# Optimization experiments

Hardware: AMD Instinct MI355X
Metric: run time of the kernel (lower is better)

Reference implementation:

```python
import jax, jax.numpy as jnp
import numpy as np
import math

B, N, DMODEL, H = 8, 1024, 256, 8
HEAD_DIM = DMODEL // H


def setup_inputs() -> dict:
    key = jax.random.key(0)
    ks = jax.random.split(key, 8)
    x = jax.random.normal(ks[0], (B, N, DMODEL), dtype=jnp.float32)
    # symmetric-ish nonnegative pairwise distances
    adj = jax.random.uniform(ks[1], (B, N, N), dtype=jnp.float32) * 10.0
    mask = jax.random.uniform(ks[2], (B, N)) < 0.9  # bool, mostly valid nodes
    W_qkv = jax.random.normal(ks[3], (DMODEL, 3 * DMODEL), dtype=jnp.float32) / math.sqrt(DMODEL)
    b_qkv = jax.random.normal(ks[4], (3 * DMODEL,), dtype=jnp.float32) * 0.01
    shifts = jnp.arange(1.0, H + 1.0, dtype=jnp.float32)  # initial_shifts
    widths = jnp.ones((H,), dtype=jnp.float32)            # initial_widths
    # self_loop_W = 1/head_dim + U(0,1), non-trainable
    self_loop_w = 1.0 / HEAD_DIM + jax.random.uniform(ks[5], (H,), dtype=jnp.float32)
    return {"x": x, "adj": adj, "mask": mask, "W_qkv": W_qkv, "b_qkv": b_qkv,
            "shifts": shifts, "widths": widths, "self_loop_w": self_loop_w}


def reference(x, adj, mask, W_qkv, b_qkv, shifts, widths, self_loop_w):
    b, n, _ = x.shape
    h = shifts.shape[0]
    d = W_qkv.shape[1] // (3 * h)
    qkv = (x @ W_qkv + b_qkv).reshape(b, n, 3, h, d)
    qkv = jnp.transpose(qkv, (2, 0, 3, 1, 4))  # [3, B, H, N, D]
    Q, K, V = qkv[0], qkv[1], qkv[2]
    scores = jnp.einsum('bhnd,bhmd->bhnm', Q, K) / jnp.sqrt(jnp.float32(d))
    # Gaussian moire focus on adjacency distances, per head
    sh = shifts.reshape(1, h, 1, 1)
    w = jnp.maximum(widths, 0.5).reshape(1, h, 1, 1)
    moire = jnp.exp(-((adj[:, None, :, :] - sh) ** 2) / w)
    adjusted = scores + jnp.log(jnp.maximum(moire, 1e-6))
    eye = jnp.eye(n, dtype=adjusted.dtype)  # [N, N]
    adjusted = adjusted + eye * self_loop_w.reshape(1, h, 1, 1)
    mask2d = (mask[:, :, None] & mask[:, None, :])[:, None, :, :]  # [B,1,N,N]
    adjusted = jnp.where(mask2d, adjusted, jnp.float32(-1000000.0))
    attn = jax.nn.softmax(adjusted, axis=-1)
    out = jnp.einsum('bhnm,bhmd->bhnd', attn, V)
    return jnp.transpose(out, (0, 2, 1, 3)).reshape(b, n, h * d)
```

## Files before the change

kernel.cpp:

```cpp
#include <hip/hip_runtime.h>

#define BB 8
#define NN 1024
#define DM 256
#define HH 8
#define HD 32
#define TC 768

typedef __bf16 bf16x8 __attribute__((ext_vector_type(8)));
typedef __bf16 bf16x4 __attribute__((ext_vector_type(4)));
typedef float  f32x4  __attribute__((ext_vector_type(4)));

__global__ __launch_bounds__(256, 4) void qkv_gemm(
    const float* __restrict__ x, const float* __restrict__ W,
    const float* __restrict__ bias, __bf16* __restrict__ Qb,
    __bf16* __restrict__ Kb, __bf16* __restrict__ Vt)
{
  __shared__ __align__(16) char U[18432];
  __bf16* As = (__bf16*)U;
  __bf16* Bs = (__bf16*)(U + 10240);

  const int tid  = threadIdx.x;
  const int w    = tid >> 6, lane = tid & 63;
  const int n16  = lane & 15, quad = lane >> 4;
  const int m0   = blockIdx.y * 128, c0 = blockIdx.x * 64;
  const int bb   = m0 >> 10, n0 = m0 & 1023;

  const int arow = tid >> 1, ahalf = tid & 1;
  const int bc   = tid & 63, bkh = tid >> 6;

  f32x4 acc[2][4] = {};

  for (int k0 = 0; k0 < DM; k0 += 32) {
    {
      const float* xa = &x[(size_t)(m0 + arow) * DM + k0 + ahalf * 16];
      float4 f0 = *(const float4*)&xa[0];
      float4 f1 = *(const float4*)&xa[4];
      float4 f2 = *(const float4*)&xa[8];
      float4 f3 = *(const float4*)&xa[12];
      bf16x8 a0, a1;
      a0[0]=(__bf16)f0.x; a0[1]=(__bf16)f0.y; a0[2]=(__bf16)f0.z; a0[3]=(__bf16)f0.w;
      a0[4]=(__bf16)f1.x; a0[5]=(__bf16)f1.y; a0[6]=(__bf16)f1.z; a0[7]=(__bf16)f1.w;
      a1[0]=(__bf16)f2.x; a1[1]=(__bf16)f2.y; a1[2]=(__bf16)f2.z; a1[3]=(__bf16)f2.w;
      a1[4]=(__bf16)f3.x; a1[5]=(__bf16)f3.y; a1[6]=(__bf16)f3.z; a1[7]=(__bf16)f3.w;
      *(bf16x8*)&As[arow*40 + ahalf*16]     = a0;
      *(bf16x8*)&As[arow*40 + ahalf*16 + 8] = a1;
    }
    {
      bf16x8 bv;
      #pragma unroll
      for (int j = 0; j < 8; ++j)
        bv[j] = (__bf16)W[(size_t)(k0 + bkh*8 + j) * TC + c0 + bc];
      *(bf16x8*)&Bs[bc*40 + bkh*8] = bv;
    }
    __syncthreads();
    bf16x8 af0 = *(const bf16x8*)&As[(w*32 + n16)*40 + quad*8];
    bf16x8 af1 = *(const bf16x8*)&As[(w*32 + 16 + n16)*40 + quad*8];
    #pragma unroll
    for (int cb = 0; cb < 4; ++cb) {
      bf16x8 bf = *(const bf16x8*)&Bs[(cb*16 + n16)*40 + quad*8];
      acc[0][cb] = __builtin_amdgcn_mfma_f32_16x16x32_bf16(af0, bf, acc[0][cb], 0, 0, 0);
      acc[1][cb] = __builtin_amdgcn_mfma_f32_16x16x32_bf16(af1, bf, acc[1][cb], 0, 0, 0);
    }
    __syncthreads();
  }

  float bv[4];
  #pragma unroll
  for (int cb = 0; cb < 4; ++cb) bv[cb] = bias[c0 + cb*16 + n16];

  if (c0 < 512) {
    __bf16* Ct = (__bf16*)U;
    #pragma unroll
    for (int cb = 0; cb < 4; ++cb)
      #pragma unroll
      for (int mb = 0; mb < 2; ++mb)
        #pragma unroll
        for (int r = 0; r < 4; ++r)
          Ct[(w*32 + mb*16 + quad*4 + r)*72 + cb*16 + n16] =
              (__bf16)(acc[mb][cb][r] + bv[cb]);
    __syncthreads();
    const int chunk = tid & 3, hh = (tid >> 2) & 1, rbase = tid >> 3;
    const int c_head = c0 + hh*32;
    const int h = (c_head >> 5) & 7;
    __bf16* base = (c_head >> 8) ? Kb : Qb;
    #pragma unroll
    for (int it = 0; it < 4; ++it) {
      int rl = rbase + it*32;
      bf16x8 v = *(const bf16x8*)&Ct[rl*72 + hh*32 + chunk*8];
      *(bf16x8*)&base[((size_t)((bb*HH + h)*NN + n0 + rl))*HD + chunk*8] = v;
    }
  } else {
    __bf16* CtT = (__bf16*)U;
    #pragma unroll
    for (int cb = 0; cb < 4; ++cb)
      #pragma unroll
      for (int mb = 0; mb < 2; ++mb) {
        bf16x4 t;
        #pragma unroll
        for (int r = 0; r < 4; ++r) t[r] = (__bf16)(acc[mb][cb][r] + bv[cb]);
        *(bf16x4*)&CtT[(cb*16 + n16)*136 + w*32 + mb*16 + quad*4] = t;
      }
    __syncthreads();
    const int col = tid >> 2, sg = tid & 3;
    const int c = c0 + col;
    const int h = (c >> 5) & 7, dd = c & 31;
    __bf16* dst = &Vt[((size_t)((bb*HH + h)*HD + dd))*NN + n0 + sg*32];
    const __bf16* srcp = &CtT[col*136 + sg*32];
    #pragma unroll
    for (int q2 = 0; q2 < 4; ++q2)
      *(bf16x8*)&dst[q2*8] = *(const bf16x8*)&srcp[q2*8];
  }
}

template <int NJT, bool SPLIT>
__global__ __launch_bounds__(256, 4) void attn_kernel(
    const __bf16* __restrict__ Q, const __bf16* __restrict__ K,
    const __bf16* __restrict__ Vt, const float* __restrict__ adj,
    const int* __restrict__ mask, const float* __restrict__ shifts,
    const float* __restrict__ widths, const float* __restrict__ slw,
    float* __restrict__ out, float* __restrict__ Opart,
    float* __restrict__ lpart)
{
  __shared__ __align__(16) char U[9216];
  __bf16 (*Qs)[40] = (__bf16(*)[40])U;
  __bf16 (*Ps)[72] = (__bf16(*)[72])U;
  __shared__ __align__(16) __bf16 Ks[2][64][40];
  __shared__ __align__(16) __bf16 Vts[2][32][72];

  const int tid  = threadIdx.x;
  const int w    = tid >> 6, lane = tid & 63;
  const int n16  = lane & 15, quad = lane >> 4;
  const int bh   = blockIdx.x >> 4, qt = blockIdx.x & 15;
  const int part = blockIdx.y;
  const int b    = bh >> 3, h = bh & 7;
  const int q0   = qt * 64;
  const int jbase = part * NJT * 64;

  const float L2E   = 1.4426950408889634f;
  const float sh    = shifts[h];
  const float ninvw = -L2E / fmaxf(widths[h], 0.5f);
  const float slv   = slw[h] * L2E;
  const float scl   = 0.17677669529663687f * L2E;
  const float LGEPS = -19.931568569324174f;
  const float MASKV = -28.0f;

  const int srow = tid >> 2, sseg = tid & 3;
  const int vd   = tid >> 3, vsg  = tid & 7;

  {
    const __bf16* Qg = Q + (size_t)(bh*NN + q0)*HD;
    *(bf16x8*)&Qs[srow][sseg*8] = *(const bf16x8*)&Qg[srow*HD + sseg*8];
  }
  const __bf16* Kg = K + (size_t)bh*NN*HD;
  const __bf16* Vg = Vt + (size_t)bh*HD*NN;
  {
    *(bf16x8*)&Ks[0][srow][sseg*8] =
        *(const bf16x8*)&Kg[(jbase + srow)*HD + sseg*8];
    *(bf16x8*)&Vts[0][vd][vsg*8] =
        *(const bf16x8*)&Vg[(size_t)vd*NN + jbase + vsg*8];
  }
  int mq[4];
  #pragma unroll
  for (int r = 0; r < 4; ++r) mq[r] = mask[b*NN + q0 + w*16 + quad*4 + r];
  __syncthreads();
  const bf16x8 qf = *(const bf16x8*)&Qs[w*16 + n16][quad*8];
  __syncthreads();

  const f32x4 zero = {0.f, 0.f, 0.f, 0.f};
  float l_r[4] = {0.f, 0.f, 0.f, 0.f};
  f32x4 o0 = zero, o1 = zero;

  const float* adjRow = adj + ((size_t)(b*NN + q0 + w*16 + quad*4))*NN;
  const int*   mrow   = mask + b*NN;

  #pragma unroll 2
  for (int jtl = 0; jtl < NJT; ++jtl) {
    const int cur = jtl & 1;
    const int j0  = jbase + jtl * 64;

    bf16x8 kn, vn;
    if (jtl < NJT - 1) {
      kn = *(const bf16x8*)&Kg[(j0 + 64 + srow)*HD + sseg*8];
      vn = *(const bf16x8*)&Vg[(size_t)vd*NN + j0 + 64 + vsg*8];
    }

    int mj[4];
    #pragma unroll
    for (int cb = 0; cb < 4; ++cb) mj[cb] = mrow[j0 + cb*16 + n16];
    float av[4][4];
    #pragma unroll
    for (int r = 0; r < 4; ++r)
      #pragma unroll
      for (int cb = 0; cb < 4; ++cb)
        av[r][cb] = adjRow[(size_t)r*NN + j0 + cb*16 + n16];

    f32x4 s[4];
    #pragma unroll
    for (int cb = 0; cb < 4; ++cb) {
      bf16x8 kf = *(const bf16x8*)&Ks[cur][cb*16 + n16][quad*8];
      s[cb] = __builtin_amdgcn_mfma_f32_16x16x32_bf16(qf, kf, zero, 0, 0, 0);
    }

    const bool diagtile = ((part * NJT + jtl) == qt);
    #pragma unroll
    for (int r = 0; r < 4; ++r) {
      const int rowl = w*16 + quad*4 + r;
      #pragma unroll
      for (int cb = 0; cb < 4; ++cb) {
        float d   = av[r][cb] - sh;
        float mo  = fmaxf(d*d*ninvw, LGEPS);
        float val = fmaf(s[cb][r], scl, mo);
        if (diagtile && (cb*16 + n16 == rowl)) val += slv;
        bool ok = (mq[r] != 0) && (mj[cb] != 0);
        val = ok ? val : MASKV;
        float p = __builtin_amdgcn_exp2f(val);
        l_r[r] += p;
        Ps[rowl][cb*16 + n16] = (__bf16)p;
      }
    }

    bf16x8 a0  = *(const bf16x8*)&Ps[w*16 + n16][quad*8];
    bf16x8 a1  = *(const bf16x8*)&Ps[w*16 + n16][32 + quad*8];
    bf16x8 b00 = *(const bf16x8*)&Vts[cur][n16][quad*8];
    bf16x8 b01 = *(const bf16x8*)&Vts[cur][n16][32 + quad*8];
    bf16x8 b10 = *(const bf16x8*)&Vts[cur][16 + n16][quad*8];
    bf16x8 b11 = *(const bf16x8*)&Vts[cur][16 + n16][32 + quad*8];
    o0 = __builtin_amdgcn_mfma_f32_16x16x32_bf16(a0, b00, o0, 0, 0, 0);
    o0 = __builtin_amdgcn_mfma_f32_16x16x32_bf16(a1, b01, o0, 0, 0, 0);
    o1 = __builtin_amdgcn_mfma_f32_16x16x32_bf16(a0, b10, o1, 0, 0, 0);
    o1 = __builtin_amdgcn_mfma_f32_16x16x32_bf16(a1, b11, o1, 0, 0, 0);

    if (jtl < NJT - 1) {
      *(bf16x8*)&Ks[1 - cur][srow][sseg*8] = kn;
      *(bf16x8*)&Vts[1 - cur][vd][vsg*8]   = vn;
    }
    __syncthreads();
  }

  #pragma unroll
  for (int r = 0; r < 4; ++r) {
    float l = l_r[r];
    l += __shfl_xor(l, 1); l += __shfl_xor(l, 2);
    l += __shfl_xor(l, 4); l += __shfl_xor(l, 8);
    const int n = q0 + w*16 + quad*4 + r;
    if (SPLIT) {
      float* og = Opart + ((size_t)(part*BB*HH + bh)*NN + n)*HD;
      og[n16]      = o0[r];
      og[16 + n16] = o1[r];
      if (n16 == 0) lpart[(size_t)(part*BB*HH + bh)*NN + n] = l;
    } else {
      const float invl = 1.0f / l;
      float* og = out + ((size_t)(b*NN + n))*DM + h*HD;
      og[n16]      = o0[r] * invl;
      og[16 + n16] = o1[r] * invl;
    }
  }
}

__global__ __launch_bounds__(256) void combine_kernel(
    const float* __restrict__ Opart, const float* __restrict__ lpart,
    float* __restrict__ out)
{
  const size_t e = (size_t)blockIdx.x * 256 + threadIdx.x;
  const int c = (int)((e << 2) & 255);
  const int n = (int)((e >> 6) & 1023);
  const int b = (int)(e >> 16);
  const int h = c >> 5, d = c & 31;
  const size_t row = (size_t)(b*HH + h)*NN + n;
  const size_t i0  = row*HD + d;
  const size_t ps  = (size_t)BB*HH*NN*HD;
  const float4 a0 = *(const float4*)&Opart[i0];
  const float4 a1 = *(const float4*)&Opart[ps + i0];
  const float  l  = lpart[row] + lpart[(size_t)BB*HH*NN + row];
  const float invl = 1.0f / l;
  float4 o = {(a0.x + a1.x)*invl, (a0.y + a1.y)*invl,
              (a0.z + a1.z)*invl, (a0.w + a1.w)*invl};
  *(float4*)&out[((size_t)(b*NN + n))*DM + c] = o;
}

extern "C" void kernel_launch(void* const* d_in, const int* in_sizes, int n_in,
                              void* d_out, int out_size, void* d_ws, size_t ws_size,
                              hipStream_t stream) {
  const float* x      = (const float*)d_in[0];
  const float* adj    = (const float*)d_in[1];
  const int*   mask   = (const int*)d_in[2];
  const float* W      = (const float*)d_in[3];
  const float* bias   = (const float*)d_in[4];
  const float* shifts = (const float*)d_in[5];
  const float* widths = (const float*)d_in[6];
  const float* slwp   = (const float*)d_in[7];
  float* out = (float*)d_out;

  const size_t BHND = (size_t)BB*HH*NN*HD;
  __bf16* Qb = (__bf16*)d_ws;
  __bf16* Kb = Qb + BHND;
  __bf16* Vt = Kb + BHND;
  float*  Opart = (float*)((char*)d_ws + 3*BHND*sizeof(__bf16));
  float*  lpart = Opart + 2*BHND;
  const size_t need = 3*BHND*2 + 2*BHND*4 + 2*(size_t)BB*HH*NN*4;

  qkv_gemm<<<dim3(TC/64, (BB*NN)/128), 256, 0, stream>>>(x, W, bias, Qb, Kb, Vt);

  if (ws_size >= need) {
    attn_kernel<8, true><<<dim3(BB*HH*(NN/64), 2), 256, 0, stream>>>(
        Qb, Kb, Vt, adj, mask, shifts, widths, slwp, out, Opart, lpart);
    combine_kernel<<<(int)(BHND/4/256), 256, 0, stream>>>(Opart, lpart, out);
  } else {
    attn_kernel<16, false><<<dim3(BB*HH*(NN/64), 1), 256, 0, stream>>>(
        Qb, Kb, Vt, adj, mask, shifts, widths, slwp, out, Opart, lpart);
  }
}
```

Before: 151.8 us.

## Single-buffer K/V tiles, raise occupancy, remap blocks head-major for adj reuse

Drops double-buffered K/V shared tiles in favour of single buffers guarded by two barriers per iteration. The launch-bounds occupancy hint goes from 4 to 8 blocks, and the unroll-2 pragma is removed. The grid becomes 1D and head-major so that blocks sharing the same adjacency rows (same batch and query tile, different heads) are spread out differently in time. The intent is more waves to hide adj memory latency and better L2 reuse of adj across heads, at the cost of an extra barrier and register pressure.

```diff
diff --git a/kernel.cpp b/kernel.cpp
--- a/kernel.cpp
+++ b/kernel.cpp
@@ -114,7 +114,7 @@
 }
 
 template <int NJT, bool SPLIT>
-__global__ __launch_bounds__(256, 4) void attn_kernel(
+__global__ __launch_bounds__(256, 8) void attn_kernel(
     const __bf16* __restrict__ Q, const __bf16* __restrict__ K,
     const __bf16* __restrict__ Vt, const float* __restrict__ adj,
     const int* __restrict__ mask, const float* __restrict__ shifts,
@@ -125,15 +125,20 @@
   __shared__ __align__(16) char U[9216];
   __bf16 (*Qs)[40] = (__bf16(*)[40])U;
   __bf16 (*Ps)[72] = (__bf16(*)[72])U;
-  __shared__ __align__(16) __bf16 Ks[2][64][40];
-  __shared__ __align__(16) __bf16 Vts[2][32][72];
-
+  __shared__ __align__(16) __bf16 Ks[64][40];
+  __shared__ __align__(16) __bf16 Vts[32][72];
+
+  constexpr int P = 16 / NJT;
   const int tid  = threadIdx.x;
   const int w    = tid >> 6, lane = tid & 63;
   const int n16  = lane & 15, quad = lane >> 4;
-  const int bh   = blockIdx.x >> 4, qt = blockIdx.x & 15;
-  const int part = blockIdx.y;
-  const int b    = bh >> 3, h = bh & 7;
+  const int idx  = blockIdx.x;
+  const int h    = idx / (128 * P);
+  const int rem  = idx - h * (128 * P);
+  const int part = rem & (P - 1);
+  const int bqt  = rem / P;
+  const int b    = bqt >> 4, qt = bqt & 15;
+  const int bh   = b * HH + h;
   const int q0   = qt * 64;
   const int jbase = part * NJT * 64;
 
@@ -148,16 +153,15 @@
   const int srow = tid >> 2, sseg = tid & 3;
   const int vd   = tid >> 3, vsg  = tid & 7;
 
+  const __bf16* Kg = K + (size_t)bh*NN*HD;
+  const __bf16* Vg = Vt + (size_t)bh*HD*NN;
+
   {
     const __bf16* Qg = Q + (size_t)(bh*NN + q0)*HD;
     *(bf16x8*)&Qs[srow][sseg*8] = *(const bf16x8*)&Qg[srow*HD + sseg*8];
-  }
-  const __bf16* Kg = K + (size_t)bh*NN*HD;
-  const __bf16* Vg = Vt + (size_t)bh*HD*NN;
-  {
-    *(bf16x8*)&Ks[0][srow][sseg*8] =
+    *(bf16x8*)&Ks[srow][sseg*8] =
         *(const bf16x8*)&Kg[(jbase + srow)*HD + sseg*8];
-    *(bf16x8*)&Vts[0][vd][vsg*8] =
+    *(bf16x8*)&Vts[vd][vsg*8] =
         *(const bf16x8*)&Vg[(size_t)vd*NN + jbase + vsg*8];
   }
   int mq[4];
@@ -174,10 +178,8 @@
   const float* adjRow = adj + ((size_t)(b*NN + q0 + w*16 + quad*4))*NN;
   const int*   mrow   = mask + b*NN;
 
-  #pragma unroll 2
   for (int jtl = 0; jtl < NJT; ++jtl) {
-    const int cur = jtl & 1;
-    const int j0  = jbase + jtl * 64;
+    const int j0 = jbase + jtl * 64;
 
     bf16x8 kn, vn;
     if (jtl < NJT - 1) {
@@ -198,7 +200,7 @@
     f32x4 s[4];
     #pragma unroll
     for (int cb = 0; cb < 4; ++cb) {
-      bf16x8 kf = *(const bf16x8*)&Ks[cur][cb*16 + n16][quad*8];
+      bf16x8 kf = *(const bf16x8*)&Ks[cb*16 + n16][quad*8];
       s[cb] = __builtin_amdgcn_mfma_f32_16x16x32_bf16(qf, kf, zero, 0, 0, 0);
     }
 
@@ -222,20 +224,21 @@
 
     bf16x8 a0  = *(const bf16x8*)&Ps[w*16 + n16][quad*8];
     bf16x8 a1  = *(const bf16x8*)&Ps[w*16 + n16][32 + quad*8];
-    bf16x8 b00 = *(const bf16x8*)&Vts[cur][n16][quad*8];
-    bf16x8 b01 = *(const bf16x8*)&Vts[cur][n16][32 + quad*8];
-    bf16x8 b10 = *(const bf16x8*)&Vts[cur][16 + n16][quad*8];
-    bf16x8 b11 = *(const bf16x8*)&Vts[cur][16 + n16][32 + quad*8];
+    bf16x8 b00 = *(const bf16x8*)&Vts[n16][quad*8];
+    bf16x8 b01 = *(const bf16x8*)&Vts[n16][32 + quad*8];
+    bf16x8 b10 = *(const bf16x8*)&Vts[16 + n16][quad*8];
+    bf16x8 b11 = *(const bf16x8*)&Vts[16 + n16][32 + quad*8];
     o0 = __builtin_amdgcn_mfma_f32_16x16x32_bf16(a0, b00, o0, 0, 0, 0);
     o0 = __builtin_amdgcn_mfma_f32_16x16x32_bf16(a1, b01, o0, 0, 0, 0);
     o1 = __builtin_amdgcn_mfma_f32_16x16x32_bf16(a0, b10, o1, 0, 0, 0);
     o1 = __builtin_amdgcn_mfma_f32_16x16x32_bf16(a1, b11, o1, 0, 0, 0);
 
     if (jtl < NJT - 1) {
-      *(bf16x8*)&Ks[1 - cur][srow][sseg*8] = kn;
-      *(bf16x8*)&Vts[1 - cur][vd][vsg*8]   = vn;
-    }
-    __syncthreads();
+      __syncthreads();
+      *(bf16x8*)&Ks[srow][sseg*8] = kn;
+      *(bf16x8*)&Vts[vd][vsg*8]   = vn;
+      __syncthreads();
+    }
   }
 
   #pragma unroll
@@ -303,11 +306,11 @@
   qkv_gemm<<<dim3(TC/64, (BB*NN)/128), 256, 0, stream>>>(x, W, bias, Qb, Kb, Vt);
 
   if (ws_size >= need) {
-    attn_kernel<8, true><<<dim3(BB*HH*(NN/64), 2), 256, 0, stream>>>(
+    attn_kernel<8, true><<<dim3(BB*HH*16*2), 256, 0, stream>>>(
         Qb, Kb, Vt, adj, mask, shifts, widths, slwp, out, Opart, lpart);
     combine_kernel<<<(int)(BHND/4/256), 256, 0, stream>>>(Opart, lpart, out);
   } else {
-    attn_kernel<16, false><<<dim3(BB*HH*(NN/64), 1), 256, 0, stream>>>(
+    attn_kernel<16, false><<<dim3(BB*HH*16), 256, 0, stream>>>(
         Qb, Kb, Vt, adj, mask, shifts, widths, slwp, out, Opart, lpart);
   }
 }
```

Result: slower. 177.7 us (+17.1%).

## Transpose attention MFMA layout for vectorized adj loads and prefetch adj tiles

Applied to the files above, without the earlier changes.

Swaps MFMA operand order so each lane owns one query row and four consecutive key columns, letting adjacency and mask rows be read as 16-byte vector loads instead of scalar strided loads. Adjacency values for the next tile are prefetched into registers alongside K/V. The P tile is written as bf16x4 vectors, and the output is staged through shared memory so it can be stored with coalesced float4 writes. This trades extra registers for prefetch plus an extra LDS round-trip and sync at the epilogue, aiming to cut the memory cost of streaming the large adjacency matrix.

```diff
diff --git a/kernel.cpp b/kernel.cpp
--- a/kernel.cpp
+++ b/kernel.cpp
@@ -10,6 +10,7 @@
 typedef __bf16 bf16x8 __attribute__((ext_vector_type(8)));
 typedef __bf16 bf16x4 __attribute__((ext_vector_type(4)));
 typedef float  f32x4  __attribute__((ext_vector_type(4)));
+typedef int    i32x4  __attribute__((ext_vector_type(4)));
 
 __global__ __launch_bounds__(256, 4) void qkv_gemm(
     const float* __restrict__ x, const float* __restrict__ W,
@@ -125,6 +126,7 @@
   __shared__ __align__(16) char U[9216];
   __bf16 (*Qs)[40] = (__bf16(*)[40])U;
   __bf16 (*Ps)[72] = (__bf16(*)[72])U;
+  float  (*Os)[36] = (float(*)[36])U;
   __shared__ __align__(16) __bf16 Ks[2][64][40];
   __shared__ __align__(16) __bf16 Vts[2][32][72];
 
@@ -136,6 +138,7 @@
   const int b    = bh >> 3, h = bh & 7;
   const int q0   = qt * 64;
   const int jbase = part * NJT * 64;
+  const int ql   = w*16 + n16;
 
   const float L2E   = 1.4426950408889634f;
   const float sh    = shifts[h];
@@ -148,31 +151,33 @@
   const int srow = tid >> 2, sseg = tid & 3;
   const int vd   = tid >> 3, vsg  = tid & 7;
 
+  const __bf16* Kg = K + (size_t)bh*NN*HD;
+  const __bf16* Vg = Vt + (size_t)bh*HD*NN;
+
   {
     const __bf16* Qg = Q + (size_t)(bh*NN + q0)*HD;
     *(bf16x8*)&Qs[srow][sseg*8] = *(const bf16x8*)&Qg[srow*HD + sseg*8];
-  }
-  const __bf16* Kg = K + (size_t)bh*NN*HD;
-  const __bf16* Vg = Vt + (size_t)bh*HD*NN;
-  {
     *(bf16x8*)&Ks[0][srow][sseg*8] =
         *(const bf16x8*)&Kg[(jbase + srow)*HD + sseg*8];
     *(bf16x8*)&Vts[0][vd][vsg*8] =
         *(const bf16x8*)&Vg[(size_t)vd*NN + jbase + vsg*8];
   }
-  int mq[4];
+  const int mq = mask[b*NN + q0 + ql];
+  const float* adjRow = adj + ((size_t)(b*NN + q0 + ql))*NN;
+  const int*   mrow   = mask + b*NN;
+
+  f32x4 av[4];
   #pragma unroll
-  for (int r = 0; r < 4; ++r) mq[r] = mask[b*NN + q0 + w*16 + quad*4 + r];
+  for (int cb = 0; cb < 4; ++cb)
+    av[cb] = *(const f32x4*)&adjRow[jbase + cb*16 + quad*4];
+
   __syncthreads();
-  const bf16x8 qf = *(const bf16x8*)&Qs[w*16 + n16][quad*8];
+  const bf16x8 qf = *(const bf16x8*)&Qs[ql][quad*8];
   __syncthreads();
 
   const f32x4 zero = {0.f, 0.f, 0.f, 0.f};
-  float l_r[4] = {0.f, 0.f, 0.f, 0.f};
-  f32x4 o0 = zero, o1 = zero;
-
-  const float* adjRow = adj + ((size_t)(b*NN + q0 + w*16 + quad*4))*NN;
-  const int*   mrow   = mask + b*NN;
+  float l_acc = 0.0f;
+  f32x4 oT0 = zero, oT1 = zero;
 
   #pragma unroll 2
   for (int jtl = 0; jtl < NJT; ++jtl) {
@@ -180,81 +185,95 @@
     const int j0  = jbase + jtl * 64;
 
     bf16x8 kn, vn;
+    f32x4  avn[4];
     if (jtl < NJT - 1) {
       kn = *(const bf16x8*)&Kg[(j0 + 64 + srow)*HD + sseg*8];
       vn = *(const bf16x8*)&Vg[(size_t)vd*NN + j0 + 64 + vsg*8];
-    }
-
-    int mj[4];
-    #pragma unroll
-    for (int cb = 0; cb < 4; ++cb) mj[cb] = mrow[j0 + cb*16 + n16];
-    float av[4][4];
-    #pragma unroll
-    for (int r = 0; r < 4; ++r)
       #pragma unroll
       for (int cb = 0; cb < 4; ++cb)
-        av[r][cb] = adjRow[(size_t)r*NN + j0 + cb*16 + n16];
+        avn[cb] = *(const f32x4*)&adjRow[j0 + 64 + cb*16 + quad*4];
+    }
+
+    i32x4 mjv[4];
+    #pragma unroll
+    for (int cb = 0; cb < 4; ++cb)
+      mjv[cb] = *(const i32x4*)&mrow[j0 + cb*16 + quad*4];
 
     f32x4 s[4];
     #pragma unroll
     for (int cb = 0; cb < 4; ++cb) {
       bf16x8 kf = *(const bf16x8*)&Ks[cur][cb*16 + n16][quad*8];
-      s[cb] = __builtin_amdgcn_mfma_f32_16x16x32_bf16(qf, kf, zero, 0, 0, 0);
+      s[cb] = __builtin_amdgcn_mfma_f32_16x16x32_bf16(kf, qf, zero, 0, 0, 0);
     }
 
     const bool diagtile = ((part * NJT + jtl) == qt);
     #pragma unroll
-    for (int r = 0; r < 4; ++r) {
-      const int rowl = w*16 + quad*4 + r;
-      #pragma unroll
-      for (int cb = 0; cb < 4; ++cb) {
-        float d   = av[r][cb] - sh;
+    for (int cb = 0; cb < 4; ++cb) {
+      bf16x4 pv;
+      #pragma unroll
+      for (int r = 0; r < 4; ++r) {
+        const int jl = cb*16 + quad*4 + r;
+        float d   = av[cb][r] - sh;
         float mo  = fmaxf(d*d*ninvw, LGEPS);
         float val = fmaf(s[cb][r], scl, mo);
-        if (diagtile && (cb*16 + n16 == rowl)) val += slv;
-        bool ok = (mq[r] != 0) && (mj[cb] != 0);
+        if (diagtile && (jl == ql)) val += slv;
+        bool ok = (mq != 0) && (mjv[cb][r] != 0);
         val = ok ? val : MASKV;
         float p = __builtin_amdgcn_exp2f(val);
-        l_r[r] += p;
-        Ps[rowl][cb*16 + n16] = (__bf16)p;
+        l_acc += p;
+        pv[r] = (__bf16)p;
       }
-    }
-
-    bf16x8 a0  = *(const bf16x8*)&Ps[w*16 + n16][quad*8];
-    bf16x8 a1  = *(const bf16x8*)&Ps[w*16 + n16][32 + quad*8];
-    bf16x8 b00 = *(const bf16x8*)&Vts[cur][n16][quad*8];
-    bf16x8 b01 = *(const bf16x8*)&Vts[cur][n16][32 + quad*8];
-    bf16x8 b10 = *(const bf16x8*)&Vts[cur][16 + n16][quad*8];
-    bf16x8 b11 = *(const bf16x8*)&Vts[cur][16 + n16][32 + quad*8];
-    o0 = __builtin_amdgcn_mfma_f32_16x16x32_bf16(a0, b00, o0, 0, 0, 0);
-    o0 = __builtin_amdgcn_mfma_f32_16x16x32_bf16(a1, b01, o0, 0, 0, 0);
-    o1 = __builtin_amdgcn_mfma_f32_16x16x32_bf16(a0, b10, o1, 0, 0, 0);
-    o1 = __builtin_amdgcn_mfma_f32_16x16x32_bf16(a1, b11, o1, 0, 0, 0);
+      *(bf16x4*)&Ps[ql][cb*16 + quad*4] = pv;
+    }
+
+    bf16x8 p0   = *(const bf16x8*)&Ps[ql][quad*8];
+    bf16x8 p1   = *(const bf16x8*)&Ps[ql][32 + quad*8];
+    bf16x8 vt00 = *(const bf16x8*)&Vts[cur][n16][quad*8];
+    bf16x8 vt01 = *(const bf16x8*)&Vts[cur][n16][32 + quad*8];
+    bf16x8 vt10 = *(const bf16x8*)&Vts[cur][16 + n16][quad*8];
+    bf16x8 vt11 = *(const bf16x8*)&Vts[cur][16 + n16][32 + quad*8];
+    oT0 = __builtin_amdgcn_mfma_f32_16x16x32_bf16(vt00, p0, oT0, 0, 0, 0);
+    oT0 = __builtin_amdgcn_mfma_f32_16x16x32_bf16(vt01, p1, oT0, 0, 0, 0);
+    oT1 = __builtin_amdgcn_mfma_f32_16x16x32_bf16(vt10, p0, oT1, 0, 0, 0);
+    oT1 = __builtin_amdgcn_mfma_f32_16x16x32_bf16(vt11, p1, oT1, 0, 0, 0);
 
     if (jtl < NJT - 1) {
       *(bf16x8*)&Ks[1 - cur][srow][sseg*8] = kn;
       *(bf16x8*)&Vts[1 - cur][vd][vsg*8]   = vn;
-    }
-    __syncthreads();
-  }
+      #pragma unroll
+      for (int cb = 0; cb < 4; ++cb) av[cb] = avn[cb];
+    }
+    __syncthreads();
+  }
+
+  float l = l_acc;
+  l += __shfl_xor(l, 16);
+  l += __shfl_xor(l, 32);
+
+  if (SPLIT) {
+    if (quad == 0)
+      lpart[(size_t)(part*BB*HH + bh)*NN + q0 + ql] = l;
+  }
+  const float sc = SPLIT ? 1.0f : (1.0f / l);
 
   #pragma unroll
   for (int r = 0; r < 4; ++r) {
-    float l = l_r[r];
-    l += __shfl_xor(l, 1); l += __shfl_xor(l, 2);
-    l += __shfl_xor(l, 4); l += __shfl_xor(l, 8);
-    const int n = q0 + w*16 + quad*4 + r;
-    if (SPLIT) {
-      float* og = Opart + ((size_t)(part*BB*HH + bh)*NN + n)*HD;
-      og[n16]      = o0[r];
-      og[16 + n16] = o1[r];
-      if (n16 == 0) lpart[(size_t)(part*BB*HH + bh)*NN + n] = l;
-    } else {
-      const float invl = 1.0f / l;
-      float* og = out + ((size_t)(b*NN + n))*DM + h*HD;
-      og[n16]      = o0[r] * invl;
-      og[16 + n16] = o1[r] * invl;
-    }
+    Os[ql][quad*4 + r]      = oT0[r] * sc;
+    Os[ql][16 + quad*4 + r] = oT1[r] * sc;
+  }
+  __syncthreads();
+  const int rl = lane >> 2, sg = lane & 3;
+  const int n  = q0 + w*16 + rl;
+  f32x4 v0 = *(const f32x4*)&Os[w*16 + rl][sg*8];
+  f32x4 v1 = *(const f32x4*)&Os[w*16 + rl][sg*8 + 4];
+  if (SPLIT) {
+    float* og = Opart + ((size_t)(part*BB*HH + bh)*NN + n)*HD;
+    *(f32x4*)&og[sg*8]     = v0;
+    *(f32x4*)&og[sg*8 + 4] = v1;
+  } else {
+    float* og = out + ((size_t)(b*NN + n))*DM + h*HD;
+    *(f32x4*)&og[sg*8]     = v0;
+    *(f32x4*)&og[sg*8 + 4] = v1;
   }
 }
 
@@ -303,11 +322,11 @@
   qkv_gemm<<<dim3(TC/64, (BB*NN)/128), 256, 0, stream>>>(x, W, bias, Qb, Kb, Vt);
 
   if (ws_size >= need) {
-    attn_kernel<8, true><<<dim3(BB*HH*(NN/64), 2), 256, 0, stream>>>(
+    attn_kernel<8, true><<<dim3(BB*HH*16, 2), 256, 0, stream>>>(
         Qb, Kb, Vt, adj, mask, shifts, widths, slwp, out, Opart, lpart);
     combine_kernel<<<(int)(BHND/4/256), 256, 0, stream>>>(Opart, lpart, out);
   } else {
-    attn_kernel<16, false><<<dim3(BB*HH*(NN/64), 1), 256, 0, stream>>>(
+    attn_kernel<16, false><<<dim3(BB*HH*16, 1), 256, 0, stream>>>(
         Qb, Kb, Vt, adj, mask, shifts, widths, slwp, out, Opart, lpart);
   }
 }
```

New measurement: 166.9 us. 1.1x slower.
